# Performance work log

Hardware: AMD Instinct MI355X
Metric: run time of the kernel (lower is better)

Reference implementation:

```python
import jax, jax.numpy as jnp
import numpy as np

INNER_DIM = 256
DT_SIZE = 64
STATE_DIM = 256  # must equal INNER_DIM for the original split() to be valid
BATCH, SEQ_LEN = 2, 512


def setup_inputs() -> dict:
    key = jax.random.key(0)
    k_x, k_win, k_wdt, k_bdt = jax.random.split(key, 4)
    x = jax.random.normal(k_x, (BATCH, SEQ_LEN, INNER_DIM), dtype=jnp.float32)
    # nn.Linear(inner_dim, dt_size + 2*state_dim, bias=False); stored as [in, out] for x @ W
    W_in = jax.random.normal(k_win, (INNER_DIM, DT_SIZE + 2 * STATE_DIM), dtype=jnp.float32) / np.sqrt(INNER_DIM)
    # nn.Linear(dt_size, inner_dim) with bias
    W_dt = jax.random.normal(k_wdt, (DT_SIZE, INNER_DIM), dtype=jnp.float32) / np.sqrt(DT_SIZE)
    b_dt = jax.random.normal(k_bdt, (INNER_DIM,), dtype=jnp.float32) * 0.01
    # alpha_log = log(repeat(arange(1, N+1), 'n -> d n'))
    alpha_log = jnp.log(jnp.broadcast_to(
        jnp.arange(1, STATE_DIM + 1, dtype=jnp.float32), (INNER_DIM, STATE_DIM)))
    delta = jnp.ones((INNER_DIM,), dtype=jnp.float32)
    return {"input_tensor": x, "W_in": W_in, "W_dt": W_dt, "b_dt": b_dt,
            "alpha_log": alpha_log, "delta": delta}


def reference(input_tensor, W_in, W_dt, b_dt, alpha_log, delta):
    x = input_tensor
    alpha = -jnp.exp(alpha_log)  # [D, N]
    proj = x @ W_in  # [B, L, DT + 2D]
    dt_raw, beta, gamma = jnp.split(proj, [DT_SIZE, DT_SIZE + INNER_DIM], axis=-1)
    dt = jax.nn.softplus(dt_raw @ W_dt + b_dt)  # [B, L, D]
    # dt_a = exp(dt[...,None] * alpha) : [B, L, D, N]
    dt_a = jnp.exp(jnp.einsum('bld,dn->bldn', dt, alpha))
    # dt_b_i = dt * x outer beta : [B, L, D, N]
    dt_b_i = jnp.einsum('bld,bln->bldn', dt * x, beta)

    def step(state, inputs):
        a_t, b_t, g_t = inputs  # [B,D,N], [B,D,N], [B,N]
        state = a_t * state + b_t
        y_t = jnp.einsum('bdn,bn->bd', state, g_t)
        return state, y_t

    s0 = jnp.zeros((x.shape[0], INNER_DIM, STATE_DIM), dtype=x.dtype)
    _, ys = jax.lax.scan(step, s0, (jnp.moveaxis(dt_a, 1, 0),
                                    jnp.moveaxis(dt_b_i, 1, 0),
                                    jnp.moveaxis(gamma, 1, 0)))
    ys = jnp.moveaxis(ys, 0, 1)  # [B, L, D]
    return ys + x * delta
```

## Files before the change

### kernel.cpp

```cpp
#include <hip/hip_runtime.h>
#include <math.h>

#define DIM   256
#define NST   256
#define LSEQ  512
#define BAT   2
#define DTSZ  64
#define PCOLS 576
#define NROWS 1024

constexpr float LOG2E = 1.4426950408889634f;

__device__ __forceinline__ float fexp2(float v) {
#if __has_builtin(__builtin_amdgcn_exp2f)
    return __builtin_amdgcn_exp2f(v);
#else
    return exp2f(v);
#endif
}

__device__ __forceinline__ float softplusf(float v) {
    return (v > 20.f) ? v : log1pf(__expf(v));
}

__device__ __forceinline__ void barrier_lds_only() {
    __builtin_amdgcn_s_waitcnt(0xC07F);
    __builtin_amdgcn_s_barrier();
}

__device__ __forceinline__ unsigned pack_bg(float be, float ga) {
    unsigned ub = __float_as_uint(be);
    unsigned ug = __float_as_uint(ga);
    ub = (ub + 0x7fffu + ((ub >> 16) & 1u)) >> 16;
    ug = (ug + 0x7fffu + ((ug >> 16) & 1u)) & 0xffff0000u;
    return ub | ug;
}

__device__ __forceinline__ float rdlane(float v, int l) {
    return __uint_as_float((unsigned)__builtin_amdgcn_readlane(
        (int)__float_as_uint(v), l));
}

__global__ __launch_bounds__(576) void proj_kernel(
    const float* __restrict__ x, const float* __restrict__ W_in,
    const float* __restrict__ W_dt, const float* __restrict__ b_dt,
    unsigned* __restrict__ betgam,
    float* __restrict__ dtp, float* __restrict__ dtxp)
{
    __shared__ float Ls[4][PCOLS];
    const int tid  = threadIdx.x;
    const int lane = tid & 63;
    const int r0   = blockIdx.x * 4;

    float vA[4][4];
    #pragma unroll
    for (int r = 0; r < 4; ++r) {
        #pragma unroll
        for (int q = 0; q < 4; ++q)
            vA[r][q] = x[(r0 + r) * DIM + q * 64 + lane];
    }

    float acc[4] = {0.f, 0.f, 0.f, 0.f};
    const float* wp = W_in + tid;
    #pragma unroll
    for (int q = 0; q < 4; ++q) {
        #pragma unroll 8
        for (int kl = 0; kl < 64; ++kl) {
            const float bw = wp[(q * 64 + kl) * PCOLS];
            #pragma unroll
            for (int r = 0; r < 4; ++r)
                acc[r] = fmaf(rdlane(vA[r][q], kl), bw, acc[r]);
        }
    }

    #pragma unroll
    for (int r = 0; r < 4; ++r) Ls[r][tid] = acc[r];
    __syncthreads();

    if (tid < 256) {
        const int d = tid;
        float vD[4];
        #pragma unroll
        for (int r = 0; r < 4; ++r) vD[r] = Ls[r][lane];

        const float bd = b_dt[d];
        float accd[4] = {bd, bd, bd, bd};
        const float* wdp = W_dt + d;
        #pragma unroll 8
        for (int k = 0; k < DTSZ; ++k) {
            const float wv = wdp[k * DIM];
            #pragma unroll
            for (int r = 0; r < 4; ++r)
                accd[r] = fmaf(rdlane(vD[r], k), wv, accd[r]);
        }
        #pragma unroll
        for (int r = 0; r < 4; ++r) {
            const int row = r0 + r;
            const float sp = softplusf(accd[r]);
            const float xv = x[row * DIM + d];
            dtp[row * DIM + d]  = sp;
            dtxp[row * DIM + d] = sp * xv;
        }
    } else if (tid < 512) {
        const int n = tid - 256;
        #pragma unroll
        for (int r = 0; r < 4; ++r) {
            const float be = Ls[r][64 + n];
            const float ga = Ls[r][320 + n];
            betgam[(r0 + r) * NST + n] = pack_bg(be, ga);
        }
    }
}

__global__ __launch_bounds__(256, 2) void scan1p(
    const float* __restrict__ x,
    const float* __restrict__ alpha_log,
    const float* __restrict__ delta,
    const unsigned* __restrict__ betgam,
    const float* __restrict__ dtp,
    const float* __restrict__ dtxp,
    float* __restrict__ out)
{
    __shared__ float part[32][NST];
    __shared__ float dts[LSEQ], dxs[LSEQ], xcol[LSEQ];
    const int n = threadIdx.x;
    const int xcd  = blockIdx.x & 7;
    const int slot = blockIdx.x >> 3;
    const int b = xcd >> 2;
    const int d = slot * 4 + (xcd & 3);
    const int rb = b * LSEQ;

    #pragma unroll
    for (int it = 0; it < 2; ++it) {
        const int l = n + it * 256;
        dts[l]  = dtp [(rb + l) * DIM + d];
        dxs[l]  = dtxp[(rb + l) * DIM + d];
        xcol[l] = x   [(rb + l) * DIM + d];
    }
    const float aln = -__expf(alpha_log[d * NST + n]) * LOG2E;
    const float dv  = delta[d];
    __syncthreads();

    float s = 0.f;
    unsigned bg[8][8];
    #pragma unroll
    for (int pw = 0; pw < 6; ++pw) {
        #pragma unroll
        for (int t = 0; t < 8; ++t)
            bg[pw][t] = betgam[(rb + pw * 8 + t) * NST + n];
    }

    #pragma unroll 8
    for (int w = 0; w < 64; ++w) {
        const int cur = w & 7;
        const int pf  = (w + 6) & 7;
        if (w + 6 < 64) {
            #pragma unroll
            for (int t = 0; t < 8; ++t)
                bg[pf][t] = betgam[(rb + (w + 6) * 8 + t) * NST + n];
        }
        float4 dta = *(const float4*)&dts[w * 8];
        float4 dtb = *(const float4*)&dts[w * 8 + 4];
        float4 dxa = *(const float4*)&dxs[w * 8];
        float4 dxb = *(const float4*)&dxs[w * 8 + 4];
        const float dtw[8] = {dta.x, dta.y, dta.z, dta.w, dtb.x, dtb.y, dtb.z, dtb.w};
        const float dxw[8] = {dxa.x, dxa.y, dxa.z, dxa.w, dxb.x, dxb.y, dxb.z, dxb.w};

        const int prow = (w & 3) * 8;
        #pragma unroll
        for (int t = 0; t < 8; ++t) {
            const unsigned u = bg[cur][t];
            const float be = __uint_as_float(u << 16);
            const float ga = __uint_as_float(u & 0xffff0000u);
            float a = fexp2(dtw[t] * aln);
            s = fmaf(a, s, dxw[t] * be);
            part[prow + t][n] = s * ga;
        }

        if ((w & 3) == 3) {
            barrier_lds_only();
            const int trow = n >> 3, seg = n & 7;
            float sum = 0.f;
            #pragma unroll
            for (int k = 0; k < 32; ++k)
                sum += part[trow][seg * 32 + ((k + n) & 31)];
            sum += __shfl_xor(sum, 1);
            sum += __shfl_xor(sum, 2);
            sum += __shfl_xor(sum, 4);
            if (seg == 0) {
                const int l = (w >> 2) * 32 + trow;
                out[(rb + l) * DIM + d] = sum + xcol[l] * dv;
            }
            barrier_lds_only();
        }
    }
}

extern "C" void kernel_launch(void* const* d_in, const int* in_sizes, int n_in,
                              void* d_out, int out_size, void* d_ws, size_t ws_size,
                              hipStream_t stream) {
    const float* x         = (const float*)d_in[0];
    const float* W_in      = (const float*)d_in[1];
    const float* W_dt      = (const float*)d_in[2];
    const float* b_dt      = (const float*)d_in[3];
    const float* alpha_log = (const float*)d_in[4];
    const float* delta     = (const float*)d_in[5];
    float* out = (float*)d_out;

    unsigned* betgam = (unsigned*)d_ws;
    float* dtp  = (float*)(betgam + NROWS * NST);
    float* dtxp = dtp + NROWS * DIM;

    proj_kernel<<<NROWS / 4, 576, 0, stream>>>(x, W_in, W_dt, b_dt, betgam, dtp, dtxp);
    scan1p<<<BAT * DIM, 256, 0, stream>>>(x, alpha_log, delta, betgam, dtp, dtxp, out);
}
```

Before: 122.1 us.

## Split sequential scan into chunked three-phase parallel scan

Replaces the single per-(batch,d) sequential scan over 512 steps with a chunked scan. There are 8 chunks of 64 steps: phase 1 computes each chunk's local end state and its dt sum, a combine kernel propagates the carry across chunks, and phase 3 re-runs each chunk from its carried initial state to produce outputs. This raises grid parallelism from 512 blocks to 4096 blocks and shortens the serial dependency chain. The cost is that the exp/fma recurrence runs twice, betgam is read twice, there are two extra launches, and about 4 MB of extra workspace traffic for the chunk states.

```diff
diff --git a/kernel.cpp b/kernel.cpp
--- a/kernel.cpp
+++ b/kernel.cpp
@@ -8,6 +8,8 @@
 #define DTSZ  64
 #define PCOLS 576
 #define NROWS 1024
+#define NCH   8
+#define LCH   64
 
 constexpr float LOG2E = 1.4426950408889634f;
 
@@ -112,52 +114,137 @@
     }
 }
 
-__global__ __launch_bounds__(256, 2) void scan1p(
+__global__ __launch_bounds__(256, 4) void scan_ph1(
+    const float* __restrict__ alpha_log,
+    const unsigned* __restrict__ betgam,
+    const float* __restrict__ dtp,
+    const float* __restrict__ dtxp,
+    float* __restrict__ Ssum,
+    float* __restrict__ sumdt)
+{
+    __shared__ float dts[LCH], dxs[LCH];
+    const int n   = threadIdx.x;
+    const int idx = blockIdx.x;
+    const int d   = idx >> 4;
+    const int b   = (idx >> 3) & 1;
+    const int c   = idx & 7;
+    const int rb  = b * LSEQ + c * LCH;
+
+    if (n < LCH) {
+        dts[n] = dtp [(rb + n) * DIM + d];
+        dxs[n] = dtxp[(rb + n) * DIM + d];
+    }
+    const float aln = -__expf(alpha_log[d * NST + n]) * LOG2E;
+    __syncthreads();
+
+    if (n < 64) {
+        float v = dts[n];
+        v += __shfl_xor(v, 1);
+        v += __shfl_xor(v, 2);
+        v += __shfl_xor(v, 4);
+        v += __shfl_xor(v, 8);
+        v += __shfl_xor(v, 16);
+        v += __shfl_xor(v, 32);
+        if (n == 0) sumdt[(b * DIM + d) * NCH + c] = v;
+    }
+
+    float s = 0.f;
+    unsigned bg[8][8];
+    #pragma unroll
+    for (int pw = 0; pw < 2; ++pw) {
+        #pragma unroll
+        for (int t = 0; t < 8; ++t)
+            bg[pw][t] = betgam[(rb + pw * 8 + t) * NST + n];
+    }
+
+    #pragma unroll
+    for (int w = 0; w < 8; ++w) {
+        if (w + 2 < 8) {
+            #pragma unroll
+            for (int t = 0; t < 8; ++t)
+                bg[w + 2][t] = betgam[(rb + (w + 2) * 8 + t) * NST + n];
+        }
+        float4 dta = *(const float4*)&dts[w * 8];
+        float4 dtb = *(const float4*)&dts[w * 8 + 4];
+        float4 dxa = *(const float4*)&dxs[w * 8];
+        float4 dxb = *(const float4*)&dxs[w * 8 + 4];
+        const float dtw[8] = {dta.x, dta.y, dta.z, dta.w, dtb.x, dtb.y, dtb.z, dtb.w};
+        const float dxw[8] = {dxa.x, dxa.y, dxa.z, dxa.w, dxb.x, dxb.y, dxb.z, dxb.w};
+        #pragma unroll
+        for (int t = 0; t < 8; ++t) {
+            const unsigned u = bg[w][t];
+            const float be = __uint_as_float(u << 16);
+            float a = fexp2(dtw[t] * aln);
+            s = fmaf(a, s, dxw[t] * be);
+        }
+    }
+    Ssum[((b * DIM + d) * NCH + c) * NST + n] = s;
+}
+
+__global__ __launch_bounds__(256) void scan_comb(
+    const float* __restrict__ alpha_log,
+    const float* __restrict__ Ssum,
+    const float* __restrict__ sumdt,
+    float* __restrict__ s0buf)
+{
+    const int n = threadIdx.x;
+    const int d = blockIdx.x >> 1;
+    const int b = blockIdx.x & 1;
+    const float aln = -__expf(alpha_log[d * NST + n]) * LOG2E;
+    const float* Sp  = Ssum  + (size_t)((b * DIM + d) * NCH) * NST + n;
+    float*       s0p = s0buf + (size_t)((b * DIM + d) * NCH) * NST + n;
+    const float* sdp = sumdt + (b * DIM + d) * NCH;
+    float run = 0.f;
+    #pragma unroll
+    for (int c = 0; c < NCH; ++c) {
+        s0p[c * NST] = run;
+        run = fmaf(fexp2(aln * sdp[c]), run, Sp[c * NST]);
+    }
+}
+
+__global__ __launch_bounds__(256, 4) void scan_ph3(
     const float* __restrict__ x,
     const float* __restrict__ alpha_log,
     const float* __restrict__ delta,
     const unsigned* __restrict__ betgam,
     const float* __restrict__ dtp,
     const float* __restrict__ dtxp,
+    const float* __restrict__ s0buf,
     float* __restrict__ out)
 {
-    __shared__ float part[32][NST];
-    __shared__ float dts[LSEQ], dxs[LSEQ], xcol[LSEQ];
-    const int n = threadIdx.x;
-    const int xcd  = blockIdx.x & 7;
-    const int slot = blockIdx.x >> 3;
-    const int b = xcd >> 2;
-    const int d = slot * 4 + (xcd & 3);
-    const int rb = b * LSEQ;
-
-    #pragma unroll
-    for (int it = 0; it < 2; ++it) {
-        const int l = n + it * 256;
-        dts[l]  = dtp [(rb + l) * DIM + d];
-        dxs[l]  = dtxp[(rb + l) * DIM + d];
-        xcol[l] = x   [(rb + l) * DIM + d];
+    __shared__ float part[16][NST + 16];
+    __shared__ float dts[LCH], dxs[LCH], xcol[LCH];
+    const int n   = threadIdx.x;
+    const int idx = blockIdx.x;
+    const int d   = idx >> 4;
+    const int b   = (idx >> 3) & 1;
+    const int c   = idx & 7;
+    const int rb  = b * LSEQ + c * LCH;
+
+    if (n < LCH) {
+        dts[n]  = dtp [(rb + n) * DIM + d];
+        dxs[n]  = dtxp[(rb + n) * DIM + d];
+        xcol[n] = x   [(rb + n) * DIM + d];
     }
     const float aln = -__expf(alpha_log[d * NST + n]) * LOG2E;
     const float dv  = delta[d];
+    float s = s0buf[((size_t)(b * DIM + d) * NCH + c) * NST + n];
     __syncthreads();
 
-    float s = 0.f;
     unsigned bg[8][8];
     #pragma unroll
-    for (int pw = 0; pw < 6; ++pw) {
+    for (int pw = 0; pw < 2; ++pw) {
         #pragma unroll
         for (int t = 0; t < 8; ++t)
             bg[pw][t] = betgam[(rb + pw * 8 + t) * NST + n];
     }
 
-    #pragma unroll 8
-    for (int w = 0; w < 64; ++w) {
-        const int cur = w & 7;
-        const int pf  = (w + 6) & 7;
-        if (w + 6 < 64) {
+    #pragma unroll
+    for (int w = 0; w < 8; ++w) {
+        if (w + 2 < 8) {
             #pragma unroll
             for (int t = 0; t < 8; ++t)
-                bg[pf][t] = betgam[(rb + (w + 6) * 8 + t) * NST + n];
+                bg[w + 2][t] = betgam[(rb + (w + 2) * 8 + t) * NST + n];
         }
         float4 dta = *(const float4*)&dts[w * 8];
         float4 dtb = *(const float4*)&dts[w * 8 + 4];
@@ -166,10 +253,10 @@
         const float dtw[8] = {dta.x, dta.y, dta.z, dta.w, dtb.x, dtb.y, dtb.z, dtb.w};
         const float dxw[8] = {dxa.x, dxa.y, dxa.z, dxa.w, dxb.x, dxb.y, dxb.z, dxb.w};
 
-        const int prow = (w & 3) * 8;
+        const int prow = (w & 1) * 8;
         #pragma unroll
         for (int t = 0; t < 8; ++t) {
-            const unsigned u = bg[cur][t];
+            const unsigned u = bg[w][t];
             const float be = __uint_as_float(u << 16);
             const float ga = __uint_as_float(u & 0xffff0000u);
             float a = fexp2(dtw[t] * aln);
@@ -177,19 +264,20 @@
             part[prow + t][n] = s * ga;
         }
 
-        if ((w & 3) == 3) {
+        if (w & 1) {
             barrier_lds_only();
-            const int trow = n >> 3, seg = n & 7;
+            const int trow = n >> 4, seg = n & 15;
             float sum = 0.f;
             #pragma unroll
-            for (int k = 0; k < 32; ++k)
-                sum += part[trow][seg * 32 + ((k + n) & 31)];
+            for (int k = 0; k < 16; ++k)
+                sum += part[trow][seg * 16 + ((k + n) & 15)];
             sum += __shfl_xor(sum, 1);
             sum += __shfl_xor(sum, 2);
             sum += __shfl_xor(sum, 4);
+            sum += __shfl_xor(sum, 8);
             if (seg == 0) {
-                const int l = (w >> 2) * 32 + trow;
-                out[(rb + l) * DIM + d] = sum + xcol[l] * dv;
+                const int ll = (w >> 1) * 16 + trow;
+                out[(rb + ll) * DIM + d] = sum + xcol[ll] * dv;
             }
             barrier_lds_only();
         }
@@ -208,9 +296,14 @@
     float* out = (float*)d_out;
 
     unsigned* betgam = (unsigned*)d_ws;
-    float* dtp  = (float*)(betgam + NROWS * NST);
-    float* dtxp = dtp + NROWS * DIM;
+    float* dtp   = (float*)(betgam + NROWS * NST);
+    float* dtxp  = dtp  + NROWS * DIM;
+    float* Ssum  = dtxp + NROWS * DIM;
+    float* s0buf = Ssum + BAT * DIM * NCH * NST;
+    float* sumdt = s0buf + BAT * DIM * NCH * NST;
 
     proj_kernel<<<NROWS / 4, 576, 0, stream>>>(x, W_in, W_dt, b_dt, betgam, dtp, dtxp);
-    scan1p<<<BAT * DIM, 256, 0, stream>>>(x, alpha_log, delta, betgam, dtp, dtxp, out);
-}
+    scan_ph1 <<<BAT * DIM * NCH, 256, 0, stream>>>(alpha_log, betgam, dtp, dtxp, Ssum, sumdt);
+    scan_comb<<<BAT * DIM,       256, 0, stream>>>(alpha_log, Ssum, sumdt, s0buf);
+    scan_ph3 <<<BAT * DIM * NCH, 256, 0, stream>>>(x, alpha_log, delta, betgam, dtp, dtxp, s0buf, out);
+}
```

Result: slower. 130.2 us (+6.6%).

## Use bf16 MFMA for input projection and fuse dt projection into scan

Applied to the files above, without the earlier changes.

Replaces the readlane-based FP32 projection kernel with a bf16 MFMA 16x16x32 GEMM. Each block stages a transposed slice of W_in in LDS and computes a 32-row tile of beta/gamma, or of the raw dt columns. The dt projection (dt_raw @ W_dt + b_dt, softplus) moves into the scan kernel, where each block computes its own column from the raw dt values. This removes the dtp/dtxp round trips and puts the GEMM on matrix cores. In exchange, x and W_in are rounded to bf16 for the dt path, and each scan block recomputes a 64-wide dot product for 512 rows.

```diff
diff --git a/kernel.cpp b/kernel.cpp
--- a/kernel.cpp
+++ b/kernel.cpp
@@ -9,6 +9,9 @@
 #define PCOLS 576
 #define NROWS 1024
 
+typedef float    f32x4 __attribute__((ext_vector_type(4)));
+typedef unsigned u32x4 __attribute__((ext_vector_type(4)));
+
 constexpr float LOG2E = 1.4426950408889634f;
 
 __device__ __forceinline__ float fexp2(float v) {
@@ -36,78 +39,86 @@
     return ub | ug;
 }
 
-__device__ __forceinline__ float rdlane(float v, int l) {
-    return __uint_as_float((unsigned)__builtin_amdgcn_readlane(
-        (int)__float_as_uint(v), l));
-}
-
-__global__ __launch_bounds__(576) void proj_kernel(
+__device__ __forceinline__ unsigned short rne16(float f) {
+    unsigned u = __float_as_uint(f);
+    return (unsigned short)((u + 0x7fffu + ((u >> 16) & 1u)) >> 16);
+}
+
+__device__ __forceinline__ unsigned cvtpk(float lo, float hi) {
+    unsigned r;
+    asm("v_cvt_pk_bf16_f32 %0, %1, %2" : "=v"(r) : "v"(lo), "v"(hi));
+    return r;
+}
+
+__device__ __forceinline__ f32x4 mfma16(u32x4 a, u32x4 b, f32x4 c) {
+    asm("v_mfma_f32_16x16x32_bf16 %0, %1, %2, %0" : "+v"(c) : "v"(a), "v"(b));
+    return c;
+}
+
+__global__ __launch_bounds__(256) void proj_mfma(
     const float* __restrict__ x, const float* __restrict__ W_in,
-    const float* __restrict__ W_dt, const float* __restrict__ b_dt,
     unsigned* __restrict__ betgam,
-    float* __restrict__ dtp, float* __restrict__ dtxp)
+    float* __restrict__ draw)
 {
-    __shared__ float Ls[4][PCOLS];
+    __shared__ unsigned short Bt[64][264];
     const int tid  = threadIdx.x;
     const int lane = tid & 63;
-    const int r0   = blockIdx.x * 4;
-
-    float vA[4][4];
-    #pragma unroll
-    for (int r = 0; r < 4; ++r) {
-        #pragma unroll
-        for (int q = 0; q < 4; ++q)
-            vA[r][q] = x[(r0 + r) * DIM + q * 64 + lane];
-    }
-
-    float acc[4] = {0.f, 0.f, 0.f, 0.f};
-    const float* wp = W_in + tid;
-    #pragma unroll
-    for (int q = 0; q < 4; ++q) {
+    const int mt   = blockIdx.x / 9;
+    const int role = blockIdx.x % 9;
+
+    const int base0 = (role < 8) ? (64  + 32 * role) : 0;
+    const int base1 = (role < 8) ? (320 + 32 * role) : 32;
+    {
+        const int cl = tid & 31;
+        const int kq = tid >> 5;
         #pragma unroll 8
-        for (int kl = 0; kl < 64; ++kl) {
-            const float bw = wp[(q * 64 + kl) * PCOLS];
-            #pragma unroll
-            for (int r = 0; r < 4; ++r)
-                acc[r] = fmaf(rdlane(vA[r][q], kl), bw, acc[r]);
-        }
-    }
-
-    #pragma unroll
-    for (int r = 0; r < 4; ++r) Ls[r][tid] = acc[r];
+        for (int p = 0; p < 32; ++p) {
+            const int k = p * 8 + kq;
+            const float v0 = W_in[k * PCOLS + base0 + cl];
+            const float v1 = W_in[k * PCOLS + base1 + cl];
+            Bt[cl][k]      = rne16(v0);
+            Bt[32 + cl][k] = rne16(v1);
+        }
+    }
     __syncthreads();
 
-    if (tid < 256) {
-        const int d = tid;
-        float vD[4];
-        #pragma unroll
-        for (int r = 0; r < 4; ++r) vD[r] = Ls[r][lane];
-
-        const float bd = b_dt[d];
-        float accd[4] = {bd, bd, bd, bd};
-        const float* wdp = W_dt + d;
-        #pragma unroll 8
-        for (int k = 0; k < DTSZ; ++k) {
-            const float wv = wdp[k * DIM];
-            #pragma unroll
-            for (int r = 0; r < 4; ++r)
-                accd[r] = fmaf(rdlane(vD[r], k), wv, accd[r]);
-        }
+    const int w    = tid >> 6;
+    const int wm   = w >> 1, wn = w & 1;
+    const int row  = mt * 32 + wm * 16 + (lane & 15);
+    const int koff = (lane >> 4) * 8;
+    const float* xp = x + row * DIM + koff;
+    const unsigned short* bp1 = &Bt[16 * wn + (lane & 15)][koff];
+    const unsigned short* bp2 = &Bt[32 + 16 * wn + (lane & 15)][koff];
+
+    f32x4 acc1 = {0.f, 0.f, 0.f, 0.f};
+    f32x4 acc2 = {0.f, 0.f, 0.f, 0.f};
+    #pragma unroll
+    for (int kk = 0; kk < 8; ++kk) {
+        const float4 xa = *(const float4*)(xp + kk * 32);
+        const float4 xb = *(const float4*)(xp + kk * 32 + 4);
+        u32x4 a;
+        a.x = cvtpk(xa.x, xa.y);
+        a.y = cvtpk(xa.z, xa.w);
+        a.z = cvtpk(xb.x, xb.y);
+        a.w = cvtpk(xb.z, xb.w);
+        const u32x4 b1 = *(const u32x4*)(bp1 + kk * 32);
+        const u32x4 b2 = *(const u32x4*)(bp2 + kk * 32);
+        acc1 = mfma16(a, b1, acc1);
+        acc2 = mfma16(a, b2, acc2);
+    }
+
+    const int rowbase = mt * 32 + wm * 16 + (lane >> 4) * 4;
+    if (role < 8) {
+        const int n = 32 * role + 16 * wn + (lane & 15);
+        #pragma unroll
+        for (int r = 0; r < 4; ++r)
+            betgam[(rowbase + r) * NST + n] = pack_bg(acc1[r], acc2[r]);
+    } else {
+        const int c1 = 16 * wn + (lane & 15);
         #pragma unroll
         for (int r = 0; r < 4; ++r) {
-            const int row = r0 + r;
-            const float sp = softplusf(accd[r]);
-            const float xv = x[row * DIM + d];
-            dtp[row * DIM + d]  = sp;
-            dtxp[row * DIM + d] = sp * xv;
-        }
-    } else if (tid < 512) {
-        const int n = tid - 256;
-        #pragma unroll
-        for (int r = 0; r < 4; ++r) {
-            const float be = Ls[r][64 + n];
-            const float ga = Ls[r][320 + n];
-            betgam[(r0 + r) * NST + n] = pack_bg(be, ga);
+            draw[(rowbase + r) * DTSZ + c1]      = acc1[r];
+            draw[(rowbase + r) * DTSZ + 32 + c1] = acc2[r];
         }
     }
 }
@@ -117,12 +128,14 @@
     const float* __restrict__ alpha_log,
     const float* __restrict__ delta,
     const unsigned* __restrict__ betgam,
-    const float* __restrict__ dtp,
-    const float* __restrict__ dtxp,
+    const float* __restrict__ draw,
+    const float* __restrict__ W_dt,
+    const float* __restrict__ b_dt,
     float* __restrict__ out)
 {
     __shared__ float part[32][NST];
     __shared__ float dts[LSEQ], dxs[LSEQ], xcol[LSEQ];
+    __shared__ float wdt[DTSZ];
     const int n = threadIdx.x;
     const int xcd  = blockIdx.x & 7;
     const int slot = blockIdx.x >> 3;
@@ -130,15 +143,35 @@
     const int d = slot * 4 + (xcd & 3);
     const int rb = b * LSEQ;
 
+    if (n < DTSZ) wdt[n] = W_dt[n * DIM + d];
     #pragma unroll
     for (int it = 0; it < 2; ++it) {
         const int l = n + it * 256;
-        dts[l]  = dtp [(rb + l) * DIM + d];
-        dxs[l]  = dtxp[(rb + l) * DIM + d];
-        xcol[l] = x   [(rb + l) * DIM + d];
+        xcol[l] = x[(rb + l) * DIM + d];
     }
     const float aln = -__expf(alpha_log[d * NST + n]) * LOG2E;
     const float dv  = delta[d];
+    const float bdv = b_dt[d];
+    __syncthreads();
+
+    #pragma unroll
+    for (int it = 0; it < 2; ++it) {
+        const int l = n + it * 256;
+        const float4* dr = (const float4*)&draw[(rb + l) * DTSZ];
+        float acc = bdv;
+        #pragma unroll
+        for (int c = 0; c < 16; ++c) {
+            const float4 v  = dr[c];
+            const float4 wv = *(const float4*)&wdt[c * 4];
+            acc = fmaf(v.x, wv.x, acc);
+            acc = fmaf(v.y, wv.y, acc);
+            acc = fmaf(v.z, wv.z, acc);
+            acc = fmaf(v.w, wv.w, acc);
+        }
+        const float sp = softplusf(acc);
+        dts[l] = sp;
+        dxs[l] = sp * xcol[l];
+    }
     __syncthreads();
 
     float s = 0.f;
@@ -208,9 +241,9 @@
     float* out = (float*)d_out;
 
     unsigned* betgam = (unsigned*)d_ws;
-    float* dtp  = (float*)(betgam + NROWS * NST);
-    float* dtxp = dtp + NROWS * DIM;
-
-    proj_kernel<<<NROWS / 4, 576, 0, stream>>>(x, W_in, W_dt, b_dt, betgam, dtp, dtxp);
-    scan1p<<<BAT * DIM, 256, 0, stream>>>(x, alpha_log, delta, betgam, dtp, dtxp, out);
-}
+    float* draw = (float*)(betgam + NROWS * NST);
+
+    proj_mfma<<<32 * 9, 256, 0, stream>>>(x, W_in, betgam, draw);
+    scan1p<<<BAT * DIM, 256, 0, stream>>>(x, alpha_log, delta, betgam,
+                                          draw, W_dt, b_dt, out);
+}
```

Result: faster. 111.3 us (-8.9%).
